# Kernel optimization log

Hardware: AMD Instinct MI355X
Metric: run time of the kernel (lower is better)

## Reference

```python
import jax, jax.numpy as jnp
import numpy as np
import math

B, N, H, OUT = 32, 2048, 256, 128
K = 6            # knn_graph k
ALPHA = 0.2      # GCN2Conv alpha (beta=1 since theta/layer are None)
NEG = 0.2        # leaky_relu negative slope in ASAP
EPS = 1e-5       # batchnorm eps
RATIOS = (0.15, 0.25, 0.5)


def _scatter_add(vals, idx, n):
    # vals [B,E] or [B,E,h], idx [B,E] -> [B,n,...]
    b, e = idx.shape
    gi = (idx + jnp.arange(b)[:, None] * n).reshape(-1)
    flat = vals.reshape((b * e,) + vals.shape[2:])
    return jax.ops.segment_sum(flat, gi, num_segments=b * n).reshape((b, n) + vals.shape[2:])


def _scatter_max(vals, idx, n):
    b, e = idx.shape
    gi = (idx + jnp.arange(b)[:, None] * n).reshape(-1)
    flat = vals.reshape((b * e,) + vals.shape[2:])
    return jax.ops.segment_max(flat, gi, num_segments=b * n).reshape((b, n) + vals.shape[2:])


def _gather(x, idx):
    # x [B,n,...] or [B,n], idx [B,E]
    if x.ndim == 3:
        return jnp.take_along_axis(x, idx[..., None], axis=1)
    return jnp.take_along_axis(x, idx, axis=1)


def _knn_undirected(pos):
    # knn_graph(pos, k=6, loop=True) then to_undirected (coalesced via `valid` mask)
    b, n, _ = pos.shape
    d2 = jnp.sum((pos[:, :, None, :] - pos[:, None, :, :]) ** 2, axis=-1)  # [B,n,n]
    _, nbr = jax.lax.top_k(-d2, K)                # self included (dist 0)
    ctr = jnp.broadcast_to(jnp.arange(n)[None, :, None], (b, n, K)).reshape(b, n * K)
    nbr = nbr.reshape(b, n * K)
    src = jnp.concatenate([nbr, ctr], axis=1)     # symmetrize
    dst = jnp.concatenate([ctr, nbr], axis=1)
    key = src * n + dst
    order = jnp.argsort(key, axis=1)
    src = jnp.take_along_axis(src, order, axis=1)
    dst = jnp.take_along_axis(dst, order, axis=1)
    key = jnp.take_along_axis(key, order, axis=1)
    valid = jnp.concatenate([jnp.ones((b, 1), bool), key[:, 1:] != key[:, :-1]], axis=1)
    return src, dst, valid


def _edge_mlp(pos, src, dst, valid, W1, b1, g, be, m, v, W2, b2):
    # relu(MLP([1,32,1])(||p_i - p_j||)); BN in eval mode; self loops replaced by 1
    d = jnp.linalg.norm(_gather(pos, src) - _gather(pos, dst), axis=-1)  # [B,E]
    t = d[..., None] @ W1 + b1                       # [B,E,32]
    t = (t - m) * jax.lax.rsqrt(v + EPS) * g + be
    t = jax.nn.relu(t)
    w = jax.nn.relu((t @ W2 + b2)[..., 0])
    w = jnp.where(src == dst, 1.0, w)                # add_remaining_self_loops fill=1
    return jnp.where(valid, w, 0.0)                  # coalesce duplicate edges


def _gcn2(x, x0, src, dst, w, Wc):
    # GCN2Conv with beta=1, shared weights: ((1-a)*A_hat x + a*x0) @ W
    n = x.shape[1]
    deg = _scatter_add(w, dst, n)
    dis = jax.lax.rsqrt(jnp.maximum(deg, 1e-12))     # deg >= 1 (self loops)
    norm = _gather(dis, src) * w * _gather(dis, dst)
    agg = _scatter_add(norm[..., None] * _gather(x, src), dst, n)
    return ((1.0 - ALPHA) * agg + ALPHA * x0) @ Wc


def _asap(x, src, dst, valid, w, kpool, Wrel, brel, Wroot, Wlin, blin, Watt, batt,
          lW1, lb1, lW2, lW3, lb3):
    n = x.shape[1]
    # gnn_intra_cluster: GraphConv (add aggregation)
    x_pool = _scatter_add(w[..., None] * _gather(x, src), dst, n) @ Wrel + brel + x @ Wroot
    mj = _gather(x_pool, src)                                    # [B,E,H]
    x_q = _scatter_max(jnp.where(valid[..., None], mj, -jnp.inf), dst, n) @ Wlin + blin
    score = (jnp.concatenate([_gather(x_q, dst), mj], axis=-1) @ Watt + batt)[..., 0]
    score = jnp.where(valid, jax.nn.leaky_relu(score, NEG), -jnp.inf)
    smax = _scatter_max(score, dst, n)
    e = jnp.where(valid, jnp.exp(score - _gather(smax, dst)), 0.0)
    att = e / _gather(_scatter_add(e, dst, n), dst)
    xn = _scatter_add(att[..., None] * _gather(x, src), dst, n)
    # LEConv fitness (no edge weights; duplicates masked)
    a = (xn @ lW1 + lb1)[..., 0]
    bb = (xn @ lW2)[..., 0]
    msg = jnp.where(valid, _gather(a, src) - _gather(bb, dst), 0.0)
    fit = jax.nn.sigmoid(_scatter_add(msg, dst, n) + (xn @ lW3 + lb3)[..., 0])
    vals, idx = jax.lax.top_k(fit, kpool)
    return _gather(xn, idx) * vals[..., None], idx


def _forward(x, pos, conv_W, eW1, eb1, ebn_g, ebn_b, ebn_m, ebn_v, eW2, eb2,
             aWrel, abrel, aWroot, aWlin, ablin, aWatt, abatt,
             leW1, leb1, leW2, leW3, leb3, gW, gb, nW, nb):
    h = None
    readouts = []
    for s in range(4):
        src, dst, valid = _knn_undirected(pos)
        w = _edge_mlp(pos, src, dst, valid, eW1[s], eb1[s], ebn_g[s], ebn_b[s],
                      ebn_m[s], ebn_v[s], eW2[s], eb2[s])
        if s in (1, 2):
            readouts.append(jnp.concatenate([jnp.mean(h, axis=1), jnp.max(h, axis=1)], axis=-1))
        hin = x if s == 0 else h
        h = jax.nn.relu(_gcn2(hin, x, src, dst, w, conv_W[s]))
        if s < 3:
            kpool = math.ceil(RATIOS[s] * h.shape[1])
            h, idx = _asap(h, src, dst, valid, w, kpool, aWrel[s], abrel[s], aWroot[s],
                           aWlin[s], ablin[s], aWatt[s], abatt[s],
                           leW1[s], leb1[s], leW2[s], leW3[s], leb3[s])
            x = _gather(x, idx)
            pos = _gather(pos, idx)
    gate = jax.nn.softmax(h @ gW + gb, axis=1)      # attentional aggregation
    gp = jnp.sum(gate * (h @ nW + nb), axis=1)      # [B,OUT]
    return jnp.concatenate([gp, readouts[1], readouts[0]], axis=-1)


def setup_inputs() -> dict:
    key = jax.random.key(0)
    ks = iter(jax.random.split(key, 40))
    def rn(shape, scale=1.0):
        return scale * jax.random.normal(next(ks), shape, dtype=jnp.float32)
    return {
        "x": rn((B, N, H)),
        "pos": rn((B, N, 3)),
        "conv_W": rn((4, H, H), H ** -0.5),
        "eW1": rn((4, 1, 32)),
        "eb1": rn((4, 32), 0.1),
        "ebn_g": 1.0 + rn((4, 32), 0.1),
        "ebn_b": rn((4, 32), 0.1),
        "ebn_m": rn((4, 32), 0.1),
        "ebn_v": jnp.ones((4, 32), jnp.float32),
        "eW2": rn((4, 32, 1), 32 ** -0.5),
        "eb2": rn((4, 1), 0.1),
        "aWrel": rn((3, H, H), H ** -0.5),
        "abrel": rn((3, H), 0.1),
        "aWroot": rn((3, H, H), H ** -0.5),
        "aWlin": rn((3, H, H), H ** -0.5),
        "ablin": rn((3, H), 0.1),
        "aWatt": rn((3, 2 * H, 1), (2 * H) ** -0.5),
        "abatt": rn((3, 1), 0.1),
        "leW1": rn((3, H, 1), H ** -0.5),
        "leb1": rn((3, 1), 0.1),
        "leW2": rn((3, H, 1), H ** -0.5),
        "leW3": rn((3, H, 1), H ** -0.5),
        "leb3": rn((3, 1), 0.1),
        "gW": rn((H, 1), H ** -0.5),
        "gb": rn((1,), 0.1),
        "nW": rn((H, OUT), H ** -0.5),
        "nb": rn((OUT,), 0.1),
    }


def reference(x, pos, conv_W, eW1, eb1, ebn_g, ebn_b, ebn_m, ebn_v, eW2, eb2,
              aWrel, abrel, aWroot, aWlin, ablin, aWatt, abatt,
              leW1, leb1, leW2, leW3, leb3, gW, gb, nW, nb):
    return _forward(x, pos, conv_W, eW1, eb1, ebn_g, ebn_b, ebn_m, ebn_v, eW2, eb2,
                    aWrel, abrel, aWroot, aWlin, ablin, aWatt, abatt,
                    leW1, leb1, leW2, leW3, leb3, gW, gb, nW, nb)
```

## Files before the change

kernel.cpp:

```cpp
#include <hip/hip_runtime.h>
#include <hip/hip_bf16.h>
#include <math.h>

#define BB 32
#define NMAX 2048
#define HD 256
#define KNN 6
#define OUTD 128

typedef __hip_bfloat16 bf16;

__global__ void k_detect(const void* __restrict__ x, int* __restrict__ flag){
  __shared__ int cnt_s;
  if (threadIdx.x==0) cnt_s=0;
  __syncthreads();
  const unsigned short* u=(const unsigned short*)x;
  int c=0;
  for (int i=threadIdx.x;i<4096;i+=256){
    int e=(u[i]>>7)&0xFF;
    if (e>=0xC0) c++;
  }
  atomicAdd(&cnt_s,c);
  __syncthreads();
  if (threadIdx.x==0) flag[0]=(cnt_s>32)?1:0;
}

__device__ __forceinline__ float loadx(const void* x, int fl, size_t idx){
  if (fl) return ((const float*)x)[idx];
  unsigned short u=((const unsigned short*)x)[idx];
  return __uint_as_float(((unsigned)u)<<16);
}

__global__ void k_cvtx(const void* __restrict__ x, const int* __restrict__ flag,
                       float* __restrict__ Hf){
  int t=blockIdx.x*256+threadIdx.x;
  Hf[t]=loadx(x,flag[0],t);
}
__global__ void k_cvtpos(const void* __restrict__ pos, const int* __restrict__ flag,
                         float* __restrict__ posF){
  int t=blockIdx.x*256+threadIdx.x;
  if (t>=BB*NMAX*3) return;
  posF[t]=loadx(pos,flag[0],t);
}
struct WTab { const void* src[25]; int cnt[25]; int dst[25]; };
__global__ void k_cvtw(WTab tab, const int* __restrict__ flag, float* __restrict__ wsW){
  int seg=blockIdx.y;
  int t=blockIdx.x*256+threadIdx.x;
  if (t>=tab.cnt[seg]) return;
  wsW[tab.dst[seg]+t]=loadx(tab.src[seg],flag[0],t);
}

__global__ void k_initcum(int* __restrict__ cum){
  int t=blockIdx.x*256+threadIdx.x;
  if (t<BB*NMAX) cum[t]=t%NMAX;
}
__global__ void k_zero2(int* __restrict__ a, int* __restrict__ b, int n){
  int t=blockIdx.x*256+threadIdx.x;
  if (t<n){ a[t]=0; b[t]=0; }
}
__global__ void k_gatherpos(const float* __restrict__ posF, const int* __restrict__ cum,
                            float* __restrict__ posf, int n){
  int t=blockIdx.x*256+threadIdx.x;
  if (t>=BB*n*3) return;
  int c=t%3, i=(t/3)%n, b=t/(3*n);
  posf[t]=posF[((size_t)b*NMAX+cum[b*NMAX+i])*3+c];
}

__global__ void k_knn(const float* __restrict__ posf, int* __restrict__ nbr, int n){
  int b=blockIdx.y;
  int i=blockIdx.x*256+threadIdx.x;
  const float* pp=posf+(size_t)b*n*3;
  double px=0.0,py=0.0,pz=0.0;
  if (i<n){ px=(double)pp[i*3]; py=(double)pp[i*3+1]; pz=(double)pp[i*3+2]; }
  double bd0=INFINITY,bd1=INFINITY,bd2=INFINITY,bd3=INFINITY,bd4=INFINITY,bd5=INFINITY;
  int   bi0=-1,bi1=-1,bi2=-1,bi3=-1,bi4=-1,bi5=-1;
  __shared__ double sx[256],sy[256],sz[256];
  for (int base=0;base<n;base+=256){
    int j=base+threadIdx.x;
    if (j<n){ sx[threadIdx.x]=(double)pp[j*3]; sy[threadIdx.x]=(double)pp[j*3+1]; sz[threadIdx.x]=(double)pp[j*3+2]; }
    __syncthreads();
    int lim=n-base; if (lim>256) lim=256;
    if (i<n){
      for (int t=0;t<lim;t++){
        double dx=__dsub_rn(px,sx[t]);
        double dy=__dsub_rn(py,sy[t]);
        double dz=__dsub_rn(pz,sz[t]);
        double d2=__dadd_rn(__dadd_rn(__dmul_rn(dx,dx),__dmul_rn(dy,dy)),__dmul_rn(dz,dz));
        if (d2<bd5){
          int id=base+t;
          if (d2<bd4){ bd5=bd4; bi5=bi4;
            if (d2<bd3){ bd4=bd3; bi4=bi3;
              if (d2<bd2){ bd3=bd2; bi3=bi2;
                if (d2<bd1){ bd2=bd1; bi2=bi1;
                  if (d2<bd0){ bd1=bd0; bi1=bi0; bd0=d2; bi0=id; }
                  else { bd1=d2; bi1=id; }
                } else { bd2=d2; bi2=id; }
              } else { bd3=d2; bi3=id; }
            } else { bd4=d2; bi4=id; }
          } else { bd5=d2; bi5=id; }
        }
      }
    }
    __syncthreads();
  }
  if (i<n){
    if (bi0<0) bi0=i; if (bi1<0) bi1=i; if (bi2<0) bi2=i;
    if (bi3<0) bi3=i; if (bi4<0) bi4=i; if (bi5<0) bi5=i;
    int* o=nbr+((size_t)b*n+i)*KNN;
    o[0]=bi0; o[1]=bi1; o[2]=bi2; o[3]=bi3; o[4]=bi4; o[5]=bi5;
  }
}

__global__ void k_edge(const float* __restrict__ posf, const int* __restrict__ nbr,
                       float* __restrict__ w1, float* __restrict__ w2,
                       unsigned char* __restrict__ val2,
                       const float* __restrict__ W1, const float* __restrict__ b1,
                       const float* __restrict__ g,  const float* __restrict__ be,
                       const float* __restrict__ m,  const float* __restrict__ v,
                       const float* __restrict__ W2, const float* __restrict__ b2p,
                       int n){
  int t=blockIdx.x*256+threadIdx.x;
  if (t>=BB*n*KNN) return;
  int k=t%KNN; int c=(t/KNN)%n; int b=t/(KNN*n);
  const int* nb=nbr+(size_t)b*n*KNN;
  int j=nb[c*KNN+k];
  bool dup=false;
  #pragma unroll
  for (int kk=0;kk<KNN;kk++) dup=dup||(nb[j*KNN+kk]==c);
  const float* pp=posf+(size_t)b*n*3;
  double dx=__dsub_rn((double)pp[c*3+0],(double)pp[j*3+0]);
  double dy=__dsub_rn((double)pp[c*3+1],(double)pp[j*3+1]);
  double dz=__dsub_rn((double)pp[c*3+2],(double)pp[j*3+2]);
  double d2=__dadd_rn(__dadd_rn(__dmul_rn(dx,dx),__dmul_rn(dy,dy)),__dmul_rn(dz,dz));
  float dd=(float)sqrt(d2);
  float wv;
  if (j==c) wv=1.0f;
  else {
    float acc=b2p[0];
    for (int q=0;q<32;q++){
      float tt=dd*W1[q]+b1[q];
      float r=1.0f/sqrtf(v[q]+1e-5f);
      tt=(tt-m[q])*r*g[q]+be[q];
      tt=fmaxf(tt,0.f);
      acc=fmaf(tt,W2[q],acc);
    }
    wv=fmaxf(acc,0.f);
  }
  w1[t]=wv;
  w2[t]=dup?0.f:wv;
  val2[t]=dup?0:1;
}

__global__ void k_csr_count(const int* __restrict__ nbr, int* __restrict__ cnt, int n){
  int t=blockIdx.x*256+threadIdx.x;
  if (t>=BB*n*KNN) return;
  int b=t/(n*KNN);
  atomicAdd(&cnt[b*n+nbr[t]],1);
}
__global__ void k_csr_scan(const int* __restrict__ cnt, int* __restrict__ offs, int n){
  int b=blockIdx.x, t=threadIdx.x;
  int L=(n+255)/256;
  __shared__ int ssum[256];
  int lo=t*L, hi=lo+L; if (hi>n) hi=n; if (lo>n) lo=n;
  int s=0;
  for (int i=lo;i<hi;i++) s+=cnt[b*n+i];
  ssum[t]=s;
  __syncthreads();
  if (t==0){
    int run=0;
    for (int q=0;q<256;q++){ int vv=ssum[q]; ssum[q]=run; run+=vv; }
  }
  __syncthreads();
  int run=ssum[t];
  for (int i=lo;i<hi;i++){ offs[b*(n+1)+i]=run; run+=cnt[b*n+i]; }
  if (lo<n && hi==n) offs[b*(n+1)+n]=run;
}
__global__ void k_csr_fill(const int* __restrict__ nbr, const int* __restrict__ offs,
                           int* __restrict__ cur, int* __restrict__ rev, int n){
  int t=blockIdx.x*256+threadIdx.x;
  if (t>=BB*n*KNN) return;
  int b=t/(n*KNN); int rem=t-b*n*KNN;
  int d=nbr[t];
  int slot=offs[b*(n+1)+d]+atomicAdd(&cur[b*n+d],1);
  if (slot<0) slot=0;
  if (slot>=n*KNN) slot=n*KNN-1;
  rev[(size_t)b*n*KNN+slot]=rem;
}
__global__ void k_csr_sort(int* __restrict__ rev, const int* __restrict__ offs, int n){
  int t=blockIdx.x*256+threadIdx.x;
  if (t>=BB*n) return;
  int b=t/n, d=t-b*n;
  size_t base=(size_t)b*n*KNN;
  int lo=offs[b*(n+1)+d], hi=offs[b*(n+1)+d+1];
  for (int a2=lo+1;a2<hi;a2++){
    int vv=rev[base+a2]; int p=a2;
    while (p>lo && rev[base+p-1]>vv){ rev[base+p]=rev[base+p-1]; p--; }
    rev[base+p]=vv;
  }
}

__global__ void k_degdis(const float* __restrict__ w1, const float* __restrict__ w2,
                         const int* __restrict__ rev, const int* __restrict__ offs,
                         float* __restrict__ dis, int n){
  int t=blockIdx.x*256+threadIdx.x;
  if (t>=BB*n) return;
  int b=t/n, d=t-b*n;
  size_t rbase=(size_t)b*n*KNN;
  float s=0.f;
  #pragma unroll
  for (int k=0;k<KNN;k++) s+=w1[(size_t)t*KNN+k];
  int lo=offs[b*(n+1)+d], hi=offs[b*(n+1)+d+1];
  for (int sl=lo;sl<hi;sl++) s+=w2[rbase+rev[rbase+sl]];
  dis[t]=1.0f/sqrtf(fmaxf(s,1e-12f));
}

template<int MODE>
__global__ void k_nbrsum(const float* __restrict__ Hin, const float* __restrict__ w1,
                         const float* __restrict__ w2, const int* __restrict__ nbr,
                         const int* __restrict__ rev, const int* __restrict__ offs,
                         const float* __restrict__ dis, const void* __restrict__ xraw,
                         const int* __restrict__ flag,
                         const int* __restrict__ cum, float* __restrict__ outp, int n){
  int wid=blockIdx.x*4+(threadIdx.x>>6);
  int lane=threadIdx.x&63;
  if (wid>=BB*n) return;
  int b=wid/n, d=wid-b*n;
  const float* Hb=Hin+(size_t)b*n*HD;
  float a0=0,a1=0,a2=0,a3=0;
  float dd=(MODE==0)?dis[wid]:0.f;
  #pragma unroll
  for (int k=0;k<KNN;k++){
    int sN=nbr[(size_t)wid*KNN+k];
    float wv=w1[(size_t)wid*KNN+k];
    float nm=(MODE==0)?dis[b*n+sN]*wv*dd:wv;
    const float* r=Hb+(size_t)sN*HD+lane;
    a0=fmaf(nm,r[0],a0); a1=fmaf(nm,r[64],a1); a2=fmaf(nm,r[128],a2); a3=fmaf(nm,r[192],a3);
  }
  size_t rbase=(size_t)b*n*KNN;
  int lo=offs[b*(n+1)+d], hi=offs[b*(n+1)+d+1];
  for (int sl=lo;sl<hi;sl++){
    int e=rev[rbase+sl];
    int sN=e/KNN;
    float wv=w2[rbase+e];
    float nm=(MODE==0)?dis[b*n+sN]*wv*dd:wv;
    const float* r=Hb+(size_t)sN*HD+lane;
    a0=fmaf(nm,r[0],a0); a1=fmaf(nm,r[64],a1); a2=fmaf(nm,r[128],a2); a3=fmaf(nm,r[192],a3);
  }
  size_t o=(size_t)wid*HD+lane;
  if (MODE==0){
    int fl=flag[0];
    size_t xb=((size_t)b*NMAX+cum[b*NMAX+d])*HD+lane;
    a0=0.8f*a0+0.2f*loadx(xraw,fl,xb);
    a1=0.8f*a1+0.2f*loadx(xraw,fl,xb+64);
    a2=0.8f*a2+0.2f*loadx(xraw,fl,xb+128);
    a3=0.8f*a3+0.2f*loadx(xraw,fl,xb+192);
  }
  outp[o]=a0; outp[o+64]=a1; outp[o+128]=a2; outp[o+192]=a3;
}

__global__ void k_mm(const float* __restrict__ A1, const float* __restrict__ B1,
                     const float* __restrict__ A2, const float* __restrict__ B2,
                     const float* __restrict__ bias, int relu,
                     float* __restrict__ Cout, int M){
  __shared__ __align__(16) float As[16][68];
  __shared__ __align__(16) float Bs[16][260];
  int tid=threadIdx.x, bm=blockIdx.x;
  int tm=tid>>4, tn=tid&15;
  float acc[4][4][4];
  #pragma unroll
  for (int b2=0;b2<4;b2++){
    #pragma unroll
    for (int i=0;i<4;i++){
      #pragma unroll
      for (int j=0;j<4;j++) acc[b2][i][j]=0.f;
    }
  }
  int l=tid*4;
  int ar=l>>4, ak=l&15;
  int arow=bm*64+ar;
  int KT = A2 ? 512 : 256;
  for (int k0=0;k0<KT;k0+=16){
    const float* Asrc=(k0<HD)?A1:A2;
    const float* Bsrc=(k0<HD)?B1:B2;
    int kc=k0&(HD-1);
    if (arow<M){
      float4 a4=*(const float4*)(Asrc+(size_t)arow*HD+kc+ak);
      As[ak][ar]=a4.x; As[ak+1][ar]=a4.y; As[ak+2][ar]=a4.z; As[ak+3][ar]=a4.w;
    } else {
      As[ak][ar]=0.f; As[ak+1][ar]=0.f; As[ak+2][ar]=0.f; As[ak+3][ar]=0.f;
    }
    #pragma unroll
    for (int c=0;c<4;c++){
      int idx=c*256+tid;
      int rkk=idx>>6, cc=(idx&63)*4;
      *(float4*)&Bs[rkk][cc]=*(const float4*)(Bsrc+(size_t)(kc+rkk)*HD+cc);
    }
    __syncthreads();
    #pragma unroll
    for (int kk=0;kk<16;kk++){
      float4 av=*(const float4*)&As[kk][tm*4];
      #pragma unroll
      for (int b2=0;b2<4;b2++){
        float4 bv=*(const float4*)&Bs[kk][b2*64+tn*4];
        acc[b2][0][0]=fmaf(av.x,bv.x,acc[b2][0][0]); acc[b2][0][1]=fmaf(av.x,bv.y,acc[b2][0][1]);
        acc[b2][0][2]=fmaf(av.x,bv.z,acc[b2][0][2]); acc[b2][0][3]=fmaf(av.x,bv.w,acc[b2][0][3]);
        acc[b2][1][0]=fmaf(av.y,bv.x,acc[b2][1][0]); acc[b2][1][1]=fmaf(av.y,bv.y,acc[b2][1][1]);
        acc[b2][1][2]=fmaf(av.y,bv.z,acc[b2][1][2]); acc[b2][1][3]=fmaf(av.y,bv.w,acc[b2][1][3]);
        acc[b2][2][0]=fmaf(av.z,bv.x,acc[b2][2][0]); acc[b2][2][1]=fmaf(av.z,bv.y,acc[b2][2][1]);
        acc[b2][2][2]=fmaf(av.z,bv.z,acc[b2][2][2]); acc[b2][2][3]=fmaf(av.z,bv.w,acc[b2][2][3]);
        acc[b2][3][0]=fmaf(av.w,bv.x,acc[b2][3][0]); acc[b2][3][1]=fmaf(av.w,bv.y,acc[b2][3][1]);
        acc[b2][3][2]=fmaf(av.w,bv.z,acc[b2][3][2]); acc[b2][3][3]=fmaf(av.w,bv.w,acc[b2][3][3]);
      }
    }
    __syncthreads();
  }
  #pragma unroll
  for (int i=0;i<4;i++){
    int grow=bm*64+tm*4+i;
    if (grow>=M) continue;
    #pragma unroll
    for (int b2=0;b2<4;b2++){
      #pragma unroll
      for (int j=0;j<4;j++){
        int gcol=b2*64+tn*4+j;
        float v=acc[b2][i][j];
        if (bias) v+=bias[gcol];
        if (relu) v=fmaxf(v,0.f);
        Cout[(size_t)grow*HD+gcol]=v;
      }
    }
  }
}

__global__ void k_va(const float* __restrict__ Wlin, const float* __restrict__ wa,
                     const float* __restrict__ blin, float* __restrict__ va){
  int i=threadIdx.x;
  float acc=0.f;
  for (int j=0;j<HD;j++) acc=fmaf(Wlin[(size_t)i*HD+j],wa[j],acc);
  va[i]=acc;
  if (i==0){
    float c=0.f;
    for (int j=0;j<HD;j++) c=fmaf(blin[j],wa[j],c);
    va[256]=c;
  }
}

__global__ void k_qd(const float* __restrict__ T, const float* __restrict__ wb,
                     const float* __restrict__ va, const int* __restrict__ nbr,
                     const int* __restrict__ rev, const int* __restrict__ offs,
                     const unsigned char* __restrict__ val2,
                     float* __restrict__ pb, float* __restrict__ qd, int n){
  int wid=blockIdx.x*4+(threadIdx.x>>6);
  int lane=threadIdx.x&63;
  if (wid>=BB*n) return;
  int b=wid/n, d=wid-b*n;
  const float* r1=T+(size_t)wid*HD;
  float p=0.f;
  for (int h=lane;h<HD;h+=64) p=fmaf(r1[h],wb[h],p);
  const float* Tb=T+(size_t)b*n*HD;
  float m0=-INFINITY,m1=-INFINITY,m2=-INFINITY,m3=-INFINITY;
  #pragma unroll
  for (int k=0;k<KNN;k++){
    int sN=nbr[(size_t)wid*KNN+k];
    const float* r=Tb+(size_t)sN*HD+lane;
    m0=fmaxf(m0,r[0]); m1=fmaxf(m1,r[64]); m2=fmaxf(m2,r[128]); m3=fmaxf(m3,r[192]);
  }
  size_t rbase=(size_t)b*n*KNN;
  int lo=offs[b*(n+1)+d], hi=offs[b*(n+1)+d+1];
  for (int sl=lo;sl<hi;sl++){
    int e=rev[rbase+sl];
    if (!val2[rbase+e]) continue;
    int sN=e/KNN;
    const float* r=Tb+(size_t)sN*HD+lane;
    m0=fmaxf(m0,r[0]); m1=fmaxf(m1,r[64]); m2=fmaxf(m2,r[128]); m3=fmaxf(m3,r[192]);
  }
  float q=va[lane]*m0+va[lane+64]*m1+va[lane+128]*m2+va[lane+192]*m3;
  #pragma unroll
  for (int o=32;o>0;o>>=1){ p+=__shfl_xor(p,o); q+=__shfl_xor(q,o); }
  if (lane==0){ pb[wid]=p; qd[wid]=q+va[256]; }
}

__global__ void k_attxn(const float* __restrict__ Hin, const float* __restrict__ pb,
                        const float* __restrict__ qd, const int* __restrict__ nbr,
                        const int* __restrict__ rev, const int* __restrict__ offs,
                        const unsigned char* __restrict__ val2, const float* __restrict__ abatt,
                        float* __restrict__ Tout, int n){
  int wid=blockIdx.x*4+(threadIdx.x>>6);
  int lane=threadIdx.x&63;
  if (wid>=BB*n) return;
  int b=wid/n, d=wid-b*n;
  float batt=abatt[0];
  float qs=qd[wid];
  const float* Hb=Hin+(size_t)b*n*HD;
  size_t rbase=(size_t)b*n*KNN;
  int lo=offs[b*(n+1)+d], hi=offs[b*(n+1)+d+1];
  float smax=-INFINITY;
  #pragma unroll
  for (int k=0;k<KNN;k++){
    int sN=nbr[(size_t)wid*KNN+k];
    float sc=qs+pb[b*n+sN]+batt;
    sc=sc>=0.f?sc:0.2f*sc;
    smax=fmaxf(smax,sc);
  }
  for (int sl=lo;sl<hi;sl++){
    int e=rev[rbase+sl];
    if (!val2[rbase+e]) continue;
    int sN=e/KNN;
    float sc=qs+pb[b*n+sN]+batt;
    sc=sc>=0.f?sc:0.2f*sc;
    smax=fmaxf(smax,sc);
  }
  float es=0.f,a0=0,a1=0,a2=0,a3=0;
  #pragma unroll
  for (int k=0;k<KNN;k++){
    int sN=nbr[(size_t)wid*KNN+k];
    float sc=qs+pb[b*n+sN]+batt;
    sc=sc>=0.f?sc:0.2f*sc;
    float e2=expf(sc-smax);
    es+=e2;
    const float* r=Hb+(size_t)sN*HD+lane;
    a0=fmaf(e2,r[0],a0); a1=fmaf(e2,r[64],a1); a2=fmaf(e2,r[128],a2); a3=fmaf(e2,r[192],a3);
  }
  for (int sl=lo;sl<hi;sl++){
    int e=rev[rbase+sl];
    if (!val2[rbase+e]) continue;
    int sN=e/KNN;
    float sc=qs+pb[b*n+sN]+batt;
    sc=sc>=0.f?sc:0.2f*sc;
    float e2=expf(sc-smax);
    es+=e2;
    const float* r=Hb+(size_t)sN*HD+lane;
    a0=fmaf(e2,r[0],a0); a1=fmaf(e2,r[64],a1); a2=fmaf(e2,r[128],a2); a3=fmaf(e2,r[192],a3);
  }
  float inv=1.f/es;
  size_t o=(size_t)wid*HD+lane;
  Tout[o]=a0*inv; Tout[o+64]=a1*inv; Tout[o+128]=a2*inv; Tout[o+192]=a3*inv;
}

__global__ void k_ledots(const float* __restrict__ T, const float* __restrict__ lW1,
                         const float* __restrict__ lb1, const float* __restrict__ lW2,
                         const float* __restrict__ lW3, const float* __restrict__ lb3,
                         float* __restrict__ av, float* __restrict__ bbv,
                         float* __restrict__ l3v, int n){
  int wid=blockIdx.x*4+(threadIdx.x>>6);
  int lane=threadIdx.x&63;
  if (wid>=BB*n) return;
  const float* r=T+(size_t)wid*HD;
  float s1=0,s2=0,s3=0;
  for (int h=lane;h<HD;h+=64){
    float vv=r[h];
    s1=fmaf(vv,lW1[h],s1); s2=fmaf(vv,lW2[h],s2); s3=fmaf(vv,lW3[h],s3);
  }
  #pragma unroll
  for (int o=32;o>0;o>>=1){ s1+=__shfl_xor(s1,o); s2+=__shfl_xor(s2,o); s3+=__shfl_xor(s3,o); }
  if (lane==0){ av[wid]=s1+lb1[0]; bbv[wid]=s2; l3v[wid]=s3+lb3[0]; }
}

__global__ void k_fit(const float* __restrict__ av, const float* __restrict__ bbv,
                      const float* __restrict__ l3v, const int* __restrict__ nbr,
                      const int* __restrict__ rev, const int* __restrict__ offs,
                      const unsigned char* __restrict__ val2, float* __restrict__ fit, int n){
  int t=blockIdx.x*256+threadIdx.x;
  if (t>=BB*n) return;
  int b=t/n, d=t-b*n;
  size_t rbase=(size_t)b*n*KNN;
  float ms=0.f; int cv=KNN;
  #pragma unroll
  for (int k=0;k<KNN;k++) ms+=av[b*n+nbr[(size_t)t*KNN+k]];
  int lo=offs[b*(n+1)+d], hi=offs[b*(n+1)+d+1];
  for (int sl=lo;sl<hi;sl++){
    int e=rev[rbase+sl];
    if (val2[rbase+e]){ ms+=av[b*n+e/KNN]; cv++; }
  }
  float z=ms-(float)cv*bbv[t]+l3v[t];
  fit[t]=1.f/(1.f+expf(-z));
}

__global__ void k_rank(const float* __restrict__ fit, float* __restrict__ svl,
                       int* __restrict__ sid, int n, int kp){
  int t=blockIdx.x*256+threadIdx.x;
  if (t>=BB*n) return;
  int b=t/n, i=t-b*n;
  float fi=fit[t];
  const float* fb=fit+(size_t)b*n;
  int rank=0;
  for (int j=0;j<n;j++){
    float fj=fb[j];
    if (fj>fi || (fj==fi && j<i)) rank++;
  }
  if (rank<kp){ svl[b*NMAX+rank]=fi; sid[b*NMAX+rank]=i; }
}

__global__ void k_pool(const float* __restrict__ T, const float* __restrict__ svl,
                       const int* __restrict__ sid, const int* __restrict__ cumA,
                       int* __restrict__ cumB, float* __restrict__ Hout, int n, int kp){
  int wid=blockIdx.x*4+(threadIdx.x>>6);
  int lane=threadIdx.x&63;
  if (wid>=BB*kp) return;
  int b=wid/kp, j=wid-b*kp;
  int srcn=sid[b*NMAX+j];
  if (srcn<0) srcn=0;
  if (srcn>=n) srcn=n-1;
  float vv=svl[b*NMAX+j];
  const float* r=T+((size_t)b*n+srcn)*HD+lane;
  float* o=Hout+((size_t)b*kp+j)*HD+lane;
  o[0]=r[0]*vv; o[64]=r[64]*vv; o[128]=r[128]*vv; o[192]=r[192]*vv;
  if (lane==0) cumB[b*NMAX+j]=cumA[b*NMAX+srcn];
}

__global__ void k_readout(const float* __restrict__ Hb, float* __restrict__ ro, int n){
  int b=blockIdx.x, h=threadIdx.x;
  const float* p=Hb+(size_t)b*n*HD+h;
  float s=0.f, m=-INFINITY;
  for (int i=0;i<n;i++){ float v=p[(size_t)i*HD]; s+=v; m=fmaxf(m,v); }
  ro[b*512+h]=s/(float)n;
  ro[b*512+256+h]=m;
}

__global__ void k_final(const float* __restrict__ Hb, const float* __restrict__ gW,
                        const float* __restrict__ gb, const float* __restrict__ nW,
                        const float* __restrict__ nbias, const float* __restrict__ ro0,
                        const float* __restrict__ ro1, float* __restrict__ outp, int n){
  int b=blockIdx.x, tid=threadIdx.x;
  int wv=tid>>6, lane=tid&63;
  __shared__ float gate[64];
  for (int i=wv;i<n;i+=4){
    const float* r=Hb+((size_t)b*n+i)*HD;
    float p=0.f;
    for (int h=lane;h<HD;h+=64) p=fmaf(r[h],gW[h],p);
    #pragma unroll
    for (int o=32;o>0;o>>=1) p+=__shfl_xor(p,o);
    if (lane==0) gate[i]=p+gb[0];
  }
  __syncthreads();
  if (tid==0){
    float mx=-INFINITY;
    for (int i=0;i<n;i++) mx=fmaxf(mx,gate[i]);
    float sm=0.f;
    for (int i=0;i<n;i++){ gate[i]=expf(gate[i]-mx); sm+=gate[i]; }
    float inv=1.f/sm;
    for (int i=0;i<n;i++) gate[i]*=inv;
  }
  __syncthreads();
  if (tid<OUTD){
    float acc=0.f;
    for (int i=0;i<n;i++){
      const float* r=Hb+((size_t)b*n+i)*HD;
      float dot=0.f;
      for (int h=0;h<HD;h++) dot=fmaf(r[h],nW[(size_t)h*OUTD+tid],dot);
      acc=fmaf(gate[i],dot+nbias[tid],acc);
    }
    outp[(size_t)b*1152+tid]=acc;
  }
  for (int q=tid;q<512;q+=256){
    outp[(size_t)b*1152+128+q]=ro1[b*512+q];
    outp[(size_t)b*1152+640+q]=ro0[b*512+q];
  }
}

extern "C" void kernel_launch(void* const* d_in, const int* in_sizes, int n_in,
                              void* d_out, int out_size, void* d_ws, size_t ws_size,
                              hipStream_t stream){
  if (n_in<27) return;
  if (in_sizes[0]!=BB*NMAX*HD || in_sizes[1]!=BB*NMAX*3) return;
  float* outp=(float*)d_out;
  (void)out_size;

  char* p=(char*)d_ws;
  auto carve=[&](size_t bytes)->char*{ char* r=p; p+=((bytes+255)/256)*256; return r; };
  float* posF=(float*)carve((size_t)BB*NMAX*3*4);
  float* posf=(float*)carve((size_t)BB*NMAX*3*4);
  float* Hbuf=(float*)carve((size_t)BB*NMAX*HD*4);
  float* Tbuf=(float*)carve((size_t)BB*NMAX*HD*4);
  static const int wcnt[25]={262144,128,128,128,128,128,128,128,4,
                             196608,768,196608,196608,768,1536,3,
                             768,3,768,768,3,256,1,32768,128};
  int woff[25]; int wtot=0;
  for (int i=0;i<25;i++){ woff[i]=wtot; wtot+=(wcnt[i]+63)&~63; }
  float* wsW=(float*)carve((size_t)wtot*4);
  int*   nbr =(int*)  carve((size_t)BB*NMAX*KNN*4);
  int*   rev =(int*)  carve((size_t)BB*NMAX*KNN*4);
  float* w1  =(float*)carve((size_t)BB*NMAX*KNN*4);
  float* w2  =(float*)carve((size_t)BB*NMAX*KNN*4);
  unsigned char* val2=(unsigned char*)carve((size_t)BB*NMAX*KNN);
  int* cnt  =(int*)carve((size_t)BB*NMAX*4);
  int* offs =(int*)carve((size_t)BB*(NMAX+1)*4);
  int* cur  =(int*)carve((size_t)BB*NMAX*4);
  float* dis=(float*)carve((size_t)BB*NMAX*4);
  float* pb =(float*)carve((size_t)BB*NMAX*4);
  float* qd =(float*)carve((size_t)BB*NMAX*4);
  float* av =(float*)carve((size_t)BB*NMAX*4);
  float* bbv=(float*)carve((size_t)BB*NMAX*4);
  float* l3v=(float*)carve((size_t)BB*NMAX*4);
  float* fit=(float*)carve((size_t)BB*NMAX*4);
  float* svl=(float*)carve((size_t)BB*NMAX*4);
  int*   sid=(int*)  carve((size_t)BB*NMAX*4);
  int* cumA =(int*)carve((size_t)BB*NMAX*4);
  int* cumB =(int*)carve((size_t)BB*NMAX*4);
  int* flag =(int*)carve(256);
  float* va =(float*)carve(272*4);
  float* ro0=(float*)carve((size_t)BB*512*4);
  float* ro1=(float*)carve((size_t)BB*512*4);
  size_t need=(size_t)(p-(char*)d_ws);
  if (ws_size<need) return;

  k_detect<<<1,256,0,stream>>>(d_in[0],flag);
  k_cvtx<<<(BB*NMAX*HD)/256,256,0,stream>>>(d_in[0],flag,Hbuf);
  k_cvtpos<<<(BB*NMAX*3+255)/256,256,0,stream>>>(d_in[1],flag,posF);
  {
    WTab tab;
    int maxc=0;
    for (int i=0;i<25;i++){ tab.src[i]=d_in[2+i]; tab.cnt[i]=wcnt[i]; tab.dst[i]=woff[i]; if (wcnt[i]>maxc) maxc=wcnt[i]; }
    k_cvtw<<<dim3((maxc+255)/256,25),256,0,stream>>>(tab,flag,wsW);
  }
  k_initcum<<<(BB*NMAX+255)/256,256,0,stream>>>(cumA);

  const int NS[4]={2048,308,77,39};
  const int KP[3]={308,77,39};

  for (int s=0;s<4;s++){
    int n=NS[s]; int M=BB*n;
    const float* wconv =wsW+woff[0]+(size_t)s*65536;
    const float* eW1p  =wsW+woff[1]+s*32;
    const float* eb1p  =wsW+woff[2]+s*32;
    const float* gp    =wsW+woff[3]+s*32;
    const float* bep   =wsW+woff[4]+s*32;
    const float* mp    =wsW+woff[5]+s*32;
    const float* vp    =wsW+woff[6]+s*32;
    const float* W2p   =wsW+woff[7]+s*32;
    const float* b2p   =wsW+woff[8]+s;
    const float* aWrelp=wsW+woff[9]+(size_t)s*65536;
    const float* abrelp=wsW+woff[10]+s*256;
    const float* aWrootp=wsW+woff[11]+(size_t)s*65536;
    const float* aWlinp=wsW+woff[12]+(size_t)s*65536;
    const float* ablinp=wsW+woff[13]+s*256;
    const float* wap   =wsW+woff[14]+s*512;
    const float* wbp   =wsW+woff[14]+s*512+256;
    const float* abattp=wsW+woff[15]+s;
    const float* leW1p =wsW+woff[16]+s*256;
    const float* leb1p =wsW+woff[17]+s;
    const float* leW2p =wsW+woff[18]+s*256;
    const float* leW3p =wsW+woff[19]+s*256;
    const float* leb3p =wsW+woff[20]+s;

    k_gatherpos<<<(BB*n*3+255)/256,256,0,stream>>>(posF,cumA,posf,n);
    k_knn<<<dim3((n+255)/256,BB),256,0,stream>>>(posf,nbr,n);
    int totE=BB*n*KNN;
    k_edge<<<(totE+255)/256,256,0,stream>>>(posf,nbr,w1,w2,val2,
        eW1p,eb1p,gp,bep,mp,vp,W2p,b2p,n);
    k_zero2<<<(BB*n+255)/256,256,0,stream>>>(cnt,cur,BB*n);
    k_csr_count<<<(totE+255)/256,256,0,stream>>>(nbr,cnt,n);
    k_csr_scan<<<BB,256,0,stream>>>(cnt,offs,n);
    k_csr_fill<<<(totE+255)/256,256,0,stream>>>(nbr,offs,cur,rev,n);
    k_csr_sort<<<(BB*n+255)/256,256,0,stream>>>(rev,offs,n);
    if (s==1) k_readout<<<BB,256,0,stream>>>(Hbuf,ro0,n);
    if (s==2) k_readout<<<BB,256,0,stream>>>(Hbuf,ro1,n);
    k_degdis<<<(BB*n+255)/256,256,0,stream>>>(w1,w2,rev,offs,dis,n);
    k_nbrsum<0><<<(BB*n+3)/4,256,0,stream>>>(Hbuf,w1,w2,nbr,rev,offs,dis,d_in[0],flag,cumA,Tbuf,n);
    k_mm<<<(M+63)/64,256,0,stream>>>(Tbuf,wconv,(const float*)nullptr,(const float*)nullptr,
                                     (const float*)nullptr,1,Hbuf,M);
    if (s<3){
      int kp=KP[s];
      k_nbrsum<1><<<(BB*n+3)/4,256,0,stream>>>(Hbuf,w1,w2,nbr,rev,offs,dis,d_in[0],flag,cumA,Tbuf,n);
      k_mm<<<(M+63)/64,256,0,stream>>>(Tbuf,aWrelp,Hbuf,aWrootp,abrelp,0,Tbuf,M);
      k_va<<<1,256,0,stream>>>(aWlinp,wap,ablinp,va);
      k_qd<<<(BB*n+3)/4,256,0,stream>>>(Tbuf,wbp,va,nbr,rev,offs,val2,pb,qd,n);
      k_attxn<<<(BB*n+3)/4,256,0,stream>>>(Hbuf,pb,qd,nbr,rev,offs,val2,abattp,Tbuf,n);
      k_ledots<<<(BB*n+3)/4,256,0,stream>>>(Tbuf,leW1p,leb1p,leW2p,leW3p,leb3p,av,bbv,l3v,n);
      k_fit<<<(BB*n+255)/256,256,0,stream>>>(av,bbv,l3v,nbr,rev,offs,val2,fit,n);
      k_rank<<<(BB*n+255)/256,256,0,stream>>>(fit,svl,sid,n,kp);
      k_pool<<<(BB*kp+3)/4,256,0,stream>>>(Tbuf,svl,sid,cumA,cumB,Hbuf,n,kp);
      { int* t=cumA; cumA=cumB; cumB=t; }
    }
  }
  k_final<<<BB,256,0,stream>>>(Hbuf,wsW+woff[21],wsW+woff[22],wsW+woff[23],wsW+woff[24],
                               ro0,ro1,outp,NS[3]);
}
```

Before: 2.268 ms.

## Split kNN search across candidate chunks and merge partial top-k lists

The kNN kernel now splits the candidate range into four chunks, each handled by its own block along a new grid dimension, and writes per-chunk top-6 distance/index lists. A new merge kernel picks the global top-6 with index tie-breaking. This raises parallelism for the fp64 distance loop, which had few blocks (n/256 × 32) on later pooled stages, at the cost of an extra launch and candidate buffer traffic.

Result: no change. 2.250 ms (-0.8%).

```diff
diff --git a/kernel.cpp b/kernel.cpp
--- a/kernel.cpp
+++ b/kernel.cpp
@@ -7,6 +7,7 @@
 #define HD 256
 #define KNN 6
 #define OUTD 128
+#define NCH 4
 
 typedef __hip_bfloat16 bf16;
 
@@ -66,20 +67,23 @@
   posf[t]=posF[((size_t)b*NMAX+cum[b*NMAX+i])*3+c];
 }
 
-__global__ void k_knn(const float* __restrict__ posf, int* __restrict__ nbr, int n){
-  int b=blockIdx.y;
+__global__ void k_knn_part(const float* __restrict__ posf, double* __restrict__ dcand,
+                           int* __restrict__ icand, int n){
+  int b=blockIdx.z, ch=blockIdx.y;
   int i=blockIdx.x*256+threadIdx.x;
   const float* pp=posf+(size_t)b*n*3;
+  int cs=(n+NCH-1)/NCH;
+  int jlo=ch*cs, jhi=jlo+cs; if (jhi>n) jhi=n;
   double px=0.0,py=0.0,pz=0.0;
   if (i<n){ px=(double)pp[i*3]; py=(double)pp[i*3+1]; pz=(double)pp[i*3+2]; }
   double bd0=INFINITY,bd1=INFINITY,bd2=INFINITY,bd3=INFINITY,bd4=INFINITY,bd5=INFINITY;
-  int   bi0=-1,bi1=-1,bi2=-1,bi3=-1,bi4=-1,bi5=-1;
+  int   bi0=0x7fffffff,bi1=0x7fffffff,bi2=0x7fffffff,bi3=0x7fffffff,bi4=0x7fffffff,bi5=0x7fffffff;
   __shared__ double sx[256],sy[256],sz[256];
-  for (int base=0;base<n;base+=256){
+  for (int base=jlo;base<jhi;base+=256){
     int j=base+threadIdx.x;
-    if (j<n){ sx[threadIdx.x]=(double)pp[j*3]; sy[threadIdx.x]=(double)pp[j*3+1]; sz[threadIdx.x]=(double)pp[j*3+2]; }
+    if (j<jhi){ sx[threadIdx.x]=(double)pp[j*3]; sy[threadIdx.x]=(double)pp[j*3+1]; sz[threadIdx.x]=(double)pp[j*3+2]; }
     __syncthreads();
-    int lim=n-base; if (lim>256) lim=256;
+    int lim=jhi-base; if (lim>256) lim=256;
     if (i<n){
       for (int t=0;t<lim;t++){
         double dx=__dsub_rn(px,sx[t]);
@@ -104,10 +108,35 @@
     __syncthreads();
   }
   if (i<n){
-    if (bi0<0) bi0=i; if (bi1<0) bi1=i; if (bi2<0) bi2=i;
-    if (bi3<0) bi3=i; if (bi4<0) bi4=i; if (bi5<0) bi5=i;
-    int* o=nbr+((size_t)b*n+i)*KNN;
-    o[0]=bi0; o[1]=bi1; o[2]=bi2; o[3]=bi3; o[4]=bi4; o[5]=bi5;
+    size_t o=(((size_t)b*NCH+ch)*n+i)*KNN;
+    dcand[o+0]=bd0; dcand[o+1]=bd1; dcand[o+2]=bd2; dcand[o+3]=bd3; dcand[o+4]=bd4; dcand[o+5]=bd5;
+    icand[o+0]=bi0; icand[o+1]=bi1; icand[o+2]=bi2; icand[o+3]=bi3; icand[o+4]=bi4; icand[o+5]=bi5;
+  }
+}
+
+__global__ void k_knn_merge(const double* __restrict__ dcand, const int* __restrict__ icand,
+                            int* __restrict__ nbr, int n){
+  int t=blockIdx.x*256+threadIdx.x;
+  if (t>=BB*n) return;
+  int b=t/n, i=t-b*n;
+  double cd[NCH*KNN]; int ci[NCH*KNN];
+  #pragma unroll
+  for (int ch=0;ch<NCH;ch++){
+    size_t o=(((size_t)b*NCH+ch)*n+i)*KNN;
+    #pragma unroll
+    for (int k=0;k<KNN;k++){ cd[ch*KNN+k]=dcand[o+k]; ci[ch*KNN+k]=icand[o+k]; }
+  }
+  int* out=nbr+(size_t)t*KNN;
+  #pragma unroll
+  for (int k=0;k<KNN;k++){
+    int best=0;
+    #pragma unroll
+    for (int q=1;q<NCH*KNN;q++){
+      bool lt=(cd[q]<cd[best])||(cd[q]==cd[best]&&ci[q]<ci[best]);
+      if (lt) best=q;
+    }
+    out[k]=ci[best];
+    cd[best]=INFINITY; ci[best]=0x7fffffff;
   }
 }
 
@@ -578,6 +607,8 @@
   int woff[25]; int wtot=0;
   for (int i=0;i<25;i++){ woff[i]=wtot; wtot+=(wcnt[i]+63)&~63; }
   float* wsW=(float*)carve((size_t)wtot*4);
+  double* dcand=(double*)carve((size_t)BB*NCH*NMAX*KNN*8);
+  int*    icand=(int*)  carve((size_t)BB*NCH*NMAX*KNN*4);
   int*   nbr =(int*)  carve((size_t)BB*NMAX*KNN*4);
   int*   rev =(int*)  carve((size_t)BB*NMAX*KNN*4);
   float* w1  =(float*)carve((size_t)BB*NMAX*KNN*4);
@@ -644,7 +675,8 @@
     const float* leb3p =wsW+woff[20]+s;
 
     k_gatherpos<<<(BB*n*3+255)/256,256,0,stream>>>(posF,cumA,posf,n);
-    k_knn<<<dim3((n+255)/256,BB),256,0,stream>>>(posf,nbr,n);
+    k_knn_part<<<dim3((n+255)/256,NCH,BB),256,0,stream>>>(posf,dcand,icand,n);
+    k_knn_merge<<<(BB*n+255)/256,256,0,stream>>>(dcand,icand,nbr,n);
     int totE=BB*n*KNN;
     k_edge<<<(totE+255)/256,256,0,stream>>>(posf,nbr,w1,w2,val2,
         eW1p,eb1p,gp,bep,mp,vp,W2p,b2p,n);
```
